# Optimization experiments

Hardware: AMD Instinct MI355X
Metric: run time of the kernel (lower is better)

Reference implementation:

```python
import jax, jax.numpy as jnp
import numpy as np

NUM_CODES = 1024
EMBED_DIM = 256
COMMITMENT_COST = 0.25


def setup_inputs() -> dict:
    key = jax.random.key(0)
    kz, kc = jax.random.split(key)
    z = jax.random.normal(kz, (131072, EMBED_DIM), dtype=jnp.float32)
    # codebook init matches nn.Embedding weight uniform_(-1/num_codes, 1/num_codes)
    codebook = jax.random.uniform(kc, (NUM_CODES, EMBED_DIM), dtype=jnp.float32,
                                  minval=-1.0 / NUM_CODES, maxval=1.0 / NUM_CODES)
    return {"z": z, "codebook": codebook}


def reference(z, codebook):
    # Squared-euclidean distances; argmin is identical to cdist (euclidean) argmin.
    z2 = jnp.sum(z * z, axis=-1, keepdims=True)            # [N, 1]
    c2 = jnp.sum(codebook * codebook, axis=-1)             # [K]
    d = z2 - 2.0 * (z @ codebook.T) + c2                   # [N, K]
    indices = jnp.argmin(d, axis=-1)                       # [N]
    zq = codebook[indices]                                 # [N, D] embedding lookup

    commitment_loss = COMMITMENT_COST * jnp.mean(
        (jax.lax.stop_gradient(zq) - z) ** 2)
    zq_st = z + jax.lax.stop_gradient(zq - z)              # straight-through
    residual = z - jax.lax.stop_gradient(zq)               # z - z_q.detach()

    counts = jnp.bincount(indices, length=NUM_CODES).astype(jnp.float32)
    avg_probs = counts / jnp.sum(counts)
    perplexity = jnp.exp(-jnp.sum(avg_probs * jnp.log(avg_probs + 1e-10)))

    return zq_st, residual, indices, commitment_loss, perplexity
```

## Files before the change

### kernel.cpp

```cpp
#include <hip/hip_runtime.h>
#include <math.h>

#define NR 131072
#define KC 1024
#define DD 256

#define ZQ_OFF  0
#define RES_OFF 33554432
#define IDX_OFF 67108864
#define LOSS_OFF 67239936
#define PERP_OFF 67239937

#define WS_CNT 0
#define WS_C2N 4096
#define WS_BSS 8192
#define WS_CBS 16384

#define MARG 5e-4f
#define CCAP 28

#define FM(x,y) __fmul_rn((x),(y))
#define FA(x,y) __fadd_rn((x),(y))

typedef __attribute__((ext_vector_type(8))) short bf16x8;
typedef __attribute__((ext_vector_type(4))) float f32x4;

static __device__ __forceinline__ unsigned short bf16h(float f) {
  unsigned int u = __float_as_uint(f);
  u += 0x7FFFu + ((u >> 16) & 1u);
  return (unsigned short)(u >> 16);
}

static __device__ __forceinline__ void glds16(const void* g, void* l) {
  __builtin_amdgcn_global_load_lds(
      (const __attribute__((address_space(1))) void*)g,
      (__attribute__((address_space(3))) void*)l, 16, 0, 0);
}

static __device__ __forceinline__ float np_sumsq128(const float* __restrict__ q) {
  float lane[16];
#pragma unroll
  for (int l = 0; l < 16; l++) {
    float s0 = FM(q[l +   0], q[l +   0]);
    float s1 = FM(q[l +  16], q[l +  16]);
    float s2 = FM(q[l +  32], q[l +  32]);
    float s3 = FM(q[l +  48], q[l +  48]);
    float s4 = FM(q[l +  64], q[l +  64]);
    float s5 = FM(q[l +  80], q[l +  80]);
    float s6 = FM(q[l +  96], q[l +  96]);
    float s7 = FM(q[l + 112], q[l + 112]);
    lane[l] = FA(FA(FA(s0, s1), FA(s2, s3)), FA(FA(s4, s5), FA(s6, s7)));
  }
#pragma unroll
  for (int h = 8; h >= 1; h >>= 1)
#pragma unroll
    for (int l = 0; l < 8; l++)
      if (l < h) lane[l] = FA(lane[l], lane[l + h]);
  return lane[0];
}

static __device__ __forceinline__ float np_sumsq256(const float* __restrict__ p) {
  return FA(np_sumsq128(p), np_sumsq128(p + 128));
}

__global__ void vqo_c2(const float* __restrict__ cb, float* __restrict__ c2n) {
  const int code = blockIdx.x * 256 + threadIdx.x;
  if (code < KC) c2n[code] = np_sumsq256(cb + (size_t)code * DD);
}

__global__ void vqo_cbsplit(const float* __restrict__ cb,
                            unsigned short* __restrict__ cbs) {
  const int g  = blockIdx.x * 256 + threadIdx.x;
  const int t  = g >> 9;
  const int gi = g & 511;
  const int kc = gi >> 6, q = (gi >> 4) & 3, c = gi & 15;
  const float* src = cb + (size_t)(t * 16 + c) * DD + kc * 32 + q * 8;
  unsigned int w[4];
#pragma unroll
  for (int p = 0; p < 4; p++)
    w[p] = (unsigned int)bf16h(src[p * 2]) |
           ((unsigned int)bf16h(src[p * 2 + 1]) << 16);
  *(uint4*)(cbs + (size_t)g * 8) = make_uint4(w[0], w[1], w[2], w[3]);
}

__global__ __launch_bounds__(256, 4) void vqo_main(
    const float* __restrict__ z, const float* __restrict__ cb,
    const unsigned short* __restrict__ cbs,
    const float* __restrict__ c2n,
    float* __restrict__ out, int* __restrict__ counts,
    double* __restrict__ bss) {
  __shared__ __align__(16) unsigned short ct[2][4096];
  __shared__ unsigned short ccode[128][CCAP];
  __shared__ float cd[128][CCAP];
  __shared__ int ccnt[128];
  __shared__ float m1row[128];
  __shared__ float z2s[128];
  __shared__ int rowidx[128];
  __shared__ double wred[4];

  const int tid = threadIdx.x, wg = blockIdx.x;
  const int wv = tid >> 6, ln = tid & 63;
  const int rl = ln & 15;
  const int qk = ln >> 4;
  const int rowg0 = wg * 128 + wv * 32 + rl;

#define STG(T, B) do {                                                        \
    _Pragma("unroll")                                                         \
    for (int u_ = 0; u_ < 2; u_++) {                                          \
      glds16(cbs + (size_t)(T) * 4096 + (size_t)((wv * 2 + u_) * 64 + ln) * 8,\
             &ct[B][(wv * 2 + u_) * 512]);                                    \
    }                                                                         \
  } while (0)

  STG(0, 0);

  bf16x8 zH0[8], zH1[8];
#pragma unroll
  for (int kc = 0; kc < 8; kc++) {
    const float4* p0 = (const float4*)(z + (size_t)rowg0 * DD + kc * 32 + qk * 8);
    const float4* p1 = (const float4*)(z + (size_t)(rowg0 + 16) * DD + kc * 32 + qk * 8);
    const float4 a0 = p0[0], b0 = p0[1];
    const float4 a1 = p1[0], b1 = p1[1];
    zH0[kc][0] = (short)bf16h(a0.x); zH0[kc][1] = (short)bf16h(a0.y);
    zH0[kc][2] = (short)bf16h(a0.z); zH0[kc][3] = (short)bf16h(a0.w);
    zH0[kc][4] = (short)bf16h(b0.x); zH0[kc][5] = (short)bf16h(b0.y);
    zH0[kc][6] = (short)bf16h(b0.z); zH0[kc][7] = (short)bf16h(b0.w);
    zH1[kc][0] = (short)bf16h(a1.x); zH1[kc][1] = (short)bf16h(a1.y);
    zH1[kc][2] = (short)bf16h(a1.z); zH1[kc][3] = (short)bf16h(a1.w);
    zH1[kc][4] = (short)bf16h(b1.x); zH1[kc][5] = (short)bf16h(b1.y);
    zH1[kc][6] = (short)bf16h(b1.z); zH1[kc][7] = (short)bf16h(b1.w);
  }

  {
    const int gg = ln >> 4, l = ln & 15;
#pragma unroll 1
    for (int g4 = 0; g4 < 8; g4++) {
      const int rlcl = wv * 32 + g4 * 4 + gg;
      const float* q = z + (size_t)(wg * 128 + rlcl) * DD;
      float blk[2];
#pragma unroll
      for (int b = 0; b < 2; b++) {
        const float* qq = q + b * 128;
        const float s0 = FM(qq[l +   0], qq[l +   0]);
        const float s1 = FM(qq[l +  16], qq[l +  16]);
        const float s2 = FM(qq[l +  32], qq[l +  32]);
        const float s3 = FM(qq[l +  48], qq[l +  48]);
        const float s4 = FM(qq[l +  64], qq[l +  64]);
        const float s5 = FM(qq[l +  80], qq[l +  80]);
        const float s6 = FM(qq[l +  96], qq[l +  96]);
        const float s7 = FM(qq[l + 112], qq[l + 112]);
        float v = FA(FA(FA(s0, s1), FA(s2, s3)), FA(FA(s4, s5), FA(s6, s7)));
#pragma unroll
        for (int h = 8; h >= 1; h >>= 1) v = FA(v, __shfl_down(v, h, 16));
        blk[b] = v;
      }
      if (l == 0) z2s[rlcl] = FA(blk[0], blk[1]);
    }
  }
  if (tid < 128) ccnt[tid] = 0;
  __syncthreads();

  const float z2v0 = z2s[wv * 32 + rl];
  const float z2v1 = z2s[wv * 32 + rl + 16];

  float m10 = INFINITY, m11 = INFINITY;
#pragma unroll 1
  for (int t = 0; t < 64; t++) {
    if (t < 63) {
      STG(t + 1, (t + 1) & 1);
      asm volatile("s_waitcnt vmcnt(2)" ::: "memory");
    } else {
      asm volatile("s_waitcnt vmcnt(0)" ::: "memory");
    }
    __builtin_amdgcn_sched_barrier(0);
    __builtin_amdgcn_s_barrier();

    const unsigned short* cbuf = ct[t & 1];
    f32x4 accA = {0.f, 0.f, 0.f, 0.f}, accB = accA;
#pragma unroll
    for (int kc = 0; kc < 8; kc++) {
      const bf16x8 aH = *(const bf16x8*)&cbuf[kc * 512 + ln * 8];
      accA = __builtin_amdgcn_mfma_f32_16x16x32_bf16(aH, zH0[kc], accA, 0, 0, 0);
      accB = __builtin_amdgcn_mfma_f32_16x16x32_bf16(aH, zH1[kc], accB, 0, 0, 0);
    }
    float dh0[4], dh1[4];
#pragma unroll
    for (int r = 0; r < 4; r++) {
      const float c2v = c2n[t * 16 + qk * 4 + r];
      dh0[r] = z2v0 - 2.f * accA[r] + c2v;
      dh1[r] = z2v1 - 2.f * accB[r] + c2v;
      m10 = fminf(m10, dh0[r]);
      m11 = fminf(m11, dh1[r]);
    }
    m10 = fminf(m10, __shfl_xor(m10, 16));
    m10 = fminf(m10, __shfl_xor(m10, 32));
    m11 = fminf(m11, __shfl_xor(m11, 16));
    m11 = fminf(m11, __shfl_xor(m11, 32));
    const int rw0 = wv * 32 + rl;
#pragma unroll
    for (int r = 0; r < 4; r++) {
      if (dh0[r] <= m10 + MARG) {
        const int s = atomicAdd(&ccnt[rw0], 1);
        if (s < CCAP) {
          ccode[rw0][s] = (unsigned short)(t * 16 + qk * 4 + r);
          cd[rw0][s] = dh0[r];
        }
      }
      if (dh1[r] <= m11 + MARG) {
        const int s = atomicAdd(&ccnt[rw0 + 16], 1);
        if (s < CCAP) {
          ccode[rw0 + 16][s] = (unsigned short)(t * 16 + qk * 4 + r);
          cd[rw0 + 16][s] = dh1[r];
        }
      }
    }
    __builtin_amdgcn_s_barrier();
  }
#undef STG

  if (qk == 0) { m1row[wv * 32 + rl] = m10; m1row[wv * 32 + rl + 16] = m11; }
  __syncthreads();

  if (tid < 128) {
    const int row = wg * 128 + tid;
    const float mf = m1row[tid] + MARG;
    const int nc = ccnt[tid];
    int best;
    if (nc > CCAP) {
      const float* zr = z + (size_t)row * DD;
      const float z2r = z2s[tid];
      float db = INFINITY; best = 0;
      for (int c = 0; c < KC; c++) {
        const float* cr = cb + (size_t)c * DD;
        float dot = 0.f;
#pragma unroll 8
        for (int k = 0; k < DD; k++) dot = __fmaf_rn(zr[k], cr[k], dot);
        const float t1 = 2.0f * dot;
        const float d = FA(FA(z2r, -t1), c2n[c]);
        if (d < db) { db = d; best = c; }
      }
    } else {
      int kept = 0, kcode = 0;
      for (int s = 0; s < nc; s++)
        if (cd[tid][s] <= mf) { kept++; kcode = ccode[tid][s]; }
      if (kept == 1) best = kcode;
      else {
        const float* zr = z + (size_t)row * DD;
        const float z2r = z2s[tid];
        float db = INFINITY; int bi = 0x7FFFFFFF;
        for (int s = 0; s < nc; s++) {
          if (cd[tid][s] > mf) continue;
          const int c = ccode[tid][s];
          const float* cr = cb + (size_t)c * DD;
          float dot = 0.f;
#pragma unroll 8
          for (int k = 0; k < DD; k++) dot = __fmaf_rn(zr[k], cr[k], dot);
          const float t1 = 2.0f * dot;
          const float d = FA(FA(z2r, -t1), c2n[c]);
          if (d < db || (d == db && c < bi)) { db = d; bi = c; }
        }
        best = bi;
      }
    }
    rowidx[tid] = best;
    atomicAdd(&counts[best], 1);
    out[IDX_OFF + row] = (float)best;
  }
  __syncthreads();

  float ss = 0.f;
#pragma unroll 1
  for (int g = 0; g < 32; g++) {
    const int rlcl = wv * 32 + g;
    const int id   = rowidx[rlcl];
    const size_t zrow = (size_t)(wg * 128 + rlcl) * DD;
    const float4 r4 = ((const float4*)(z  + zrow))[ln];
    const float4 q4 = ((const float4*)(cb + (size_t)id * DD))[ln];
    float4 stv, rsv; float dq;
    stv.x = r4.x + (q4.x - r4.x); rsv.x = r4.x - q4.x; dq = q4.x - r4.x; ss = fmaf(dq, dq, ss);
    stv.y = r4.y + (q4.y - r4.y); rsv.y = r4.y - q4.y; dq = q4.y - r4.y; ss = fmaf(dq, dq, ss);
    stv.z = r4.z + (q4.z - r4.z); rsv.z = r4.z - q4.z; dq = q4.z - r4.z; ss = fmaf(dq, dq, ss);
    stv.w = r4.w + (q4.w - r4.w); rsv.w = r4.w - q4.w; dq = q4.w - r4.w; ss = fmaf(dq, dq, ss);
    ((float4*)(out + ZQ_OFF  + zrow))[ln] = stv;
    ((float4*)(out + RES_OFF + zrow))[ln] = rsv;
  }
  double dss = (double)ss;
  for (int o = 32; o; o >>= 1) dss += __shfl_down(dss, o, 64);
  if (ln == 0) wred[wv] = dss;
  __syncthreads();
  if (tid == 0) bss[wg] = wred[0] + wred[1] + wred[2] + wred[3];
}

__global__ void vqo_final(const int* __restrict__ counts,
                          const double* __restrict__ bss,
                          float* __restrict__ out) {
  __shared__ double red[256];
  const int t = threadIdx.x;
  double s = 0.0;
  for (int i = t; i < 1024; i += 256) s += bss[i];
  red[t] = s; __syncthreads();
  for (int s2 = 128; s2 > 0; s2 >>= 1) { if (t < s2) red[t] += red[t + s2]; __syncthreads(); }
  const double ssq = red[0];
  __syncthreads();
  double h = 0.0;
  for (int c = t; c < 1024; c += 256) {
    double p = (double)counts[c] / 131072.0;
    h += p * log(p + 1e-10);
  }
  red[t] = h; __syncthreads();
  for (int s2 = 128; s2 > 0; s2 >>= 1) { if (t < s2) red[t] += red[t + s2]; __syncthreads(); }
  if (t == 0) {
    out[LOSS_OFF] = (float)(0.25 * ssq / 33554432.0);
    out[PERP_OFF] = (float)exp(-red[0]);
  }
}

extern "C" void kernel_launch(void* const* d_in, const int* in_sizes, int n_in,
                              void* d_out, int out_size, void* d_ws, size_t ws_size,
                              hipStream_t stream) {
  const float* z;
  const float* cb;
  if (in_sizes[0] == NR * DD) { z = (const float*)d_in[0]; cb = (const float*)d_in[1]; }
  else                        { cb = (const float*)d_in[0]; z = (const float*)d_in[1]; }

  float* out = (float*)d_out;
  char* ws = (char*)d_ws;
  int*            counts = (int*)(ws + WS_CNT);
  float*          c2n    = (float*)(ws + WS_C2N);
  double*         bssp   = (double*)(ws + WS_BSS);
  unsigned short* cbs    = (unsigned short*)(ws + WS_CBS);

  hipMemsetAsync(counts, 0, 4096, stream);
  vqo_c2<<<4, 256, 0, stream>>>(cb, c2n);
  vqo_cbsplit<<<128, 256, 0, stream>>>(cb, cbs);
  vqo_main<<<NR / 128, 256, 0, stream>>>(z, cb, cbs, c2n, out, counts, bssp);
  vqo_final<<<1, 256, 0, stream>>>(counts, bssp, out);
}
```

Before: 316.0 us.

## Halve rows per block to cut registers and raise occupancy

Each wave now handles 16 rows instead of 32, so each block covers 64 rows and the grid doubles to 2048 blocks. This halves the z register fragments and MFMA accumulators, and launch bounds are raised to 6 blocks per CU so more waves can hide latency. The trade-off is that every block still streams the full codebook through LDS, so codebook traffic per row doubles and each MFMA has less reuse. The candidate cap shrinks to 24 and the workspace layout moves to fit the doubled per-block partial sums.

```diff
diff --git a/kernel.cpp b/kernel.cpp
--- a/kernel.cpp
+++ b/kernel.cpp
@@ -14,10 +14,10 @@
 #define WS_CNT 0
 #define WS_C2N 4096
 #define WS_BSS 8192
-#define WS_CBS 16384
+#define WS_CBS 24576
 
 #define MARG 5e-4f
-#define CCAP 28
+#define CCAP 24
 
 #define FM(x,y) __fmul_rn((x),(y))
 #define FA(x,y) __fadd_rn((x),(y))
@@ -63,12 +63,12 @@
   return FA(np_sumsq128(p), np_sumsq128(p + 128));
 }
 
-__global__ void vqo_c2(const float* __restrict__ cb, float* __restrict__ c2n) {
+__global__ void vqp_c2(const float* __restrict__ cb, float* __restrict__ c2n) {
   const int code = blockIdx.x * 256 + threadIdx.x;
   if (code < KC) c2n[code] = np_sumsq256(cb + (size_t)code * DD);
 }
 
-__global__ void vqo_cbsplit(const float* __restrict__ cb,
+__global__ void vqp_cbsplit(const float* __restrict__ cb,
                             unsigned short* __restrict__ cbs) {
   const int g  = blockIdx.x * 256 + threadIdx.x;
   const int t  = g >> 9;
@@ -83,26 +83,27 @@
   *(uint4*)(cbs + (size_t)g * 8) = make_uint4(w[0], w[1], w[2], w[3]);
 }
 
-__global__ __launch_bounds__(256, 4) void vqo_main(
+__global__ __launch_bounds__(256, 6) void vqp_main(
     const float* __restrict__ z, const float* __restrict__ cb,
     const unsigned short* __restrict__ cbs,
     const float* __restrict__ c2n,
     float* __restrict__ out, int* __restrict__ counts,
     double* __restrict__ bss) {
   __shared__ __align__(16) unsigned short ct[2][4096];
-  __shared__ unsigned short ccode[128][CCAP];
-  __shared__ float cd[128][CCAP];
-  __shared__ int ccnt[128];
-  __shared__ float m1row[128];
-  __shared__ float z2s[128];
-  __shared__ int rowidx[128];
+  __shared__ unsigned short ccode[64][CCAP];
+  __shared__ float cd[64][CCAP];
+  __shared__ int ccnt[64];
+  __shared__ float m1row[64];
+  __shared__ float z2s[64];
+  __shared__ int rowidx[64];
   __shared__ double wred[4];
 
   const int tid = threadIdx.x, wg = blockIdx.x;
   const int wv = tid >> 6, ln = tid & 63;
   const int rl = ln & 15;
   const int qk = ln >> 4;
-  const int rowg0 = wg * 128 + wv * 32 + rl;
+  const int rw = wv * 16 + rl;
+  const int rowg = wg * 64 + rw;
 
 #define STG(T, B) do {                                                        \
     _Pragma("unroll")                                                         \
@@ -114,29 +115,23 @@
 
   STG(0, 0);
 
-  bf16x8 zH0[8], zH1[8];
+  bf16x8 zH[8];
 #pragma unroll
   for (int kc = 0; kc < 8; kc++) {
-    const float4* p0 = (const float4*)(z + (size_t)rowg0 * DD + kc * 32 + qk * 8);
-    const float4* p1 = (const float4*)(z + (size_t)(rowg0 + 16) * DD + kc * 32 + qk * 8);
+    const float4* p0 = (const float4*)(z + (size_t)rowg * DD + kc * 32 + qk * 8);
     const float4 a0 = p0[0], b0 = p0[1];
-    const float4 a1 = p1[0], b1 = p1[1];
-    zH0[kc][0] = (short)bf16h(a0.x); zH0[kc][1] = (short)bf16h(a0.y);
-    zH0[kc][2] = (short)bf16h(a0.z); zH0[kc][3] = (short)bf16h(a0.w);
-    zH0[kc][4] = (short)bf16h(b0.x); zH0[kc][5] = (short)bf16h(b0.y);
-    zH0[kc][6] = (short)bf16h(b0.z); zH0[kc][7] = (short)bf16h(b0.w);
-    zH1[kc][0] = (short)bf16h(a1.x); zH1[kc][1] = (short)bf16h(a1.y);
-    zH1[kc][2] = (short)bf16h(a1.z); zH1[kc][3] = (short)bf16h(a1.w);
-    zH1[kc][4] = (short)bf16h(b1.x); zH1[kc][5] = (short)bf16h(b1.y);
-    zH1[kc][6] = (short)bf16h(b1.z); zH1[kc][7] = (short)bf16h(b1.w);
+    zH[kc][0] = (short)bf16h(a0.x); zH[kc][1] = (short)bf16h(a0.y);
+    zH[kc][2] = (short)bf16h(a0.z); zH[kc][3] = (short)bf16h(a0.w);
+    zH[kc][4] = (short)bf16h(b0.x); zH[kc][5] = (short)bf16h(b0.y);
+    zH[kc][6] = (short)bf16h(b0.z); zH[kc][7] = (short)bf16h(b0.w);
   }
 
   {
     const int gg = ln >> 4, l = ln & 15;
 #pragma unroll 1
-    for (int g4 = 0; g4 < 8; g4++) {
-      const int rlcl = wv * 32 + g4 * 4 + gg;
-      const float* q = z + (size_t)(wg * 128 + rlcl) * DD;
+    for (int g4 = 0; g4 < 4; g4++) {
+      const int rlcl = wv * 16 + g4 * 4 + gg;
+      const float* q = z + (size_t)(wg * 64 + rlcl) * DD;
       float blk[2];
 #pragma unroll
       for (int b = 0; b < 2; b++) {
@@ -157,13 +152,12 @@
       if (l == 0) z2s[rlcl] = FA(blk[0], blk[1]);
     }
   }
-  if (tid < 128) ccnt[tid] = 0;
-  __syncthreads();
-
-  const float z2v0 = z2s[wv * 32 + rl];
-  const float z2v1 = z2s[wv * 32 + rl + 16];
-
-  float m10 = INFINITY, m11 = INFINITY;
+  if (tid < 64) ccnt[tid] = 0;
+  __syncthreads();
+
+  const float z2v = z2s[rw];
+
+  float m1 = INFINITY;
 #pragma unroll 1
   for (int t = 0; t < 64; t++) {
     if (t < 63) {
@@ -176,53 +170,40 @@
     __builtin_amdgcn_s_barrier();
 
     const unsigned short* cbuf = ct[t & 1];
-    f32x4 accA = {0.f, 0.f, 0.f, 0.f}, accB = accA;
+    f32x4 accA = {0.f, 0.f, 0.f, 0.f};
 #pragma unroll
     for (int kc = 0; kc < 8; kc++) {
       const bf16x8 aH = *(const bf16x8*)&cbuf[kc * 512 + ln * 8];
-      accA = __builtin_amdgcn_mfma_f32_16x16x32_bf16(aH, zH0[kc], accA, 0, 0, 0);
-      accB = __builtin_amdgcn_mfma_f32_16x16x32_bf16(aH, zH1[kc], accB, 0, 0, 0);
-    }
-    float dh0[4], dh1[4];
+      accA = __builtin_amdgcn_mfma_f32_16x16x32_bf16(aH, zH[kc], accA, 0, 0, 0);
+    }
+    float dh[4];
 #pragma unroll
     for (int r = 0; r < 4; r++) {
       const float c2v = c2n[t * 16 + qk * 4 + r];
-      dh0[r] = z2v0 - 2.f * accA[r] + c2v;
-      dh1[r] = z2v1 - 2.f * accB[r] + c2v;
-      m10 = fminf(m10, dh0[r]);
-      m11 = fminf(m11, dh1[r]);
-    }
-    m10 = fminf(m10, __shfl_xor(m10, 16));
-    m10 = fminf(m10, __shfl_xor(m10, 32));
-    m11 = fminf(m11, __shfl_xor(m11, 16));
-    m11 = fminf(m11, __shfl_xor(m11, 32));
-    const int rw0 = wv * 32 + rl;
+      dh[r] = z2v - 2.f * accA[r] + c2v;
+      m1 = fminf(m1, dh[r]);
+    }
+    m1 = fminf(m1, __shfl_xor(m1, 16));
+    m1 = fminf(m1, __shfl_xor(m1, 32));
 #pragma unroll
     for (int r = 0; r < 4; r++) {
-      if (dh0[r] <= m10 + MARG) {
-        const int s = atomicAdd(&ccnt[rw0], 1);
+      if (dh[r] <= m1 + MARG) {
+        const int s = atomicAdd(&ccnt[rw], 1);
         if (s < CCAP) {
-          ccode[rw0][s] = (unsigned short)(t * 16 + qk * 4 + r);
-          cd[rw0][s] = dh0[r];
+          ccode[rw][s] = (unsigned short)(t * 16 + qk * 4 + r);
+          cd[rw][s] = dh[r];
         }
       }
-      if (dh1[r] <= m11 + MARG) {
-        const int s = atomicAdd(&ccnt[rw0 + 16], 1);
-        if (s < CCAP) {
-          ccode[rw0 + 16][s] = (unsigned short)(t * 16 + qk * 4 + r);
-          cd[rw0 + 16][s] = dh1[r];
-        }
-      }
     }
     __builtin_amdgcn_s_barrier();
   }
 #undef STG
 
-  if (qk == 0) { m1row[wv * 32 + rl] = m10; m1row[wv * 32 + rl + 16] = m11; }
-  __syncthreads();
-
-  if (tid < 128) {
-    const int row = wg * 128 + tid;
+  if (qk == 0) m1row[rw] = m1;
+  __syncthreads();
+
+  if (tid < 64) {
+    const int row = wg * 64 + tid;
     const float mf = m1row[tid] + MARG;
     const int nc = ccnt[tid];
     int best;
@@ -270,10 +251,10 @@
 
   float ss = 0.f;
 #pragma unroll 1
-  for (int g = 0; g < 32; g++) {
-    const int rlcl = wv * 32 + g;
+  for (int g = 0; g < 16; g++) {
+    const int rlcl = wv * 16 + g;
     const int id   = rowidx[rlcl];
-    const size_t zrow = (size_t)(wg * 128 + rlcl) * DD;
+    const size_t zrow = (size_t)(wg * 64 + rlcl) * DD;
     const float4 r4 = ((const float4*)(z  + zrow))[ln];
     const float4 q4 = ((const float4*)(cb + (size_t)id * DD))[ln];
     float4 stv, rsv; float dq;
@@ -291,13 +272,13 @@
   if (tid == 0) bss[wg] = wred[0] + wred[1] + wred[2] + wred[3];
 }
 
-__global__ void vqo_final(const int* __restrict__ counts,
+__global__ void vqp_final(const int* __restrict__ counts,
                           const double* __restrict__ bss,
                           float* __restrict__ out) {
   __shared__ double red[256];
   const int t = threadIdx.x;
   double s = 0.0;
-  for (int i = t; i < 1024; i += 256) s += bss[i];
+  for (int i = t; i < 2048; i += 256) s += bss[i];
   red[t] = s; __syncthreads();
   for (int s2 = 128; s2 > 0; s2 >>= 1) { if (t < s2) red[t] += red[t + s2]; __syncthreads(); }
   const double ssq = red[0];
@@ -331,8 +312,8 @@
   unsigned short* cbs    = (unsigned short*)(ws + WS_CBS);
 
   hipMemsetAsync(counts, 0, 4096, stream);
-  vqo_c2<<<4, 256, 0, stream>>>(cb, c2n);
-  vqo_cbsplit<<<128, 256, 0, stream>>>(cb, cbs);
-  vqo_main<<<NR / 128, 256, 0, stream>>>(z, cb, cbs, c2n, out, counts, bssp);
-  vqo_final<<<1, 256, 0, stream>>>(counts, bssp, out);
-}
+  vqp_c2<<<4, 256, 0, stream>>>(cb, c2n);
+  vqp_cbsplit<<<128, 256, 0, stream>>>(cb, cbs);
+  vqp_main<<<NR / 64, 256, 0, stream>>>(z, cb, cbs, c2n, out, counts, bssp);
+  vqp_final<<<1, 256, 0, stream>>>(counts, bssp, out);
+}
```

After: 344.7 us. +9.1%, slower.

## Load codebook tiles directly to registers and drop LDS staging barriers

Applied to the files above, without the earlier changes.

Removes the double-buffered global_load_lds staging of the bf16 codebook tiles and the per-tile workgroup barriers. Each wave now loads its MFMA A operands straight from global (L2-resident) memory, with the loop unrolled by two so loads can overlap. The c2 norms are cached in LDS and read as a float4, and the candidate resolution is split across all four waves instead of the first 128 threads. Candidate capacity is reduced to cut LDS use. The trade-off is redundant global/L2 traffic from every wave and no explicit prefetch, and fewer candidate slots mean more rows may fall back to the full exact search.

```diff
diff --git a/kernel.cpp b/kernel.cpp
--- a/kernel.cpp
+++ b/kernel.cpp
@@ -17,7 +17,7 @@
 #define WS_CBS 16384
 
 #define MARG 5e-4f
-#define CCAP 28
+#define CCAP 24
 
 #define FM(x,y) __fmul_rn((x),(y))
 #define FA(x,y) __fadd_rn((x),(y))
@@ -29,12 +29,6 @@
   unsigned int u = __float_as_uint(f);
   u += 0x7FFFu + ((u >> 16) & 1u);
   return (unsigned short)(u >> 16);
-}
-
-static __device__ __forceinline__ void glds16(const void* g, void* l) {
-  __builtin_amdgcn_global_load_lds(
-      (const __attribute__((address_space(1))) void*)g,
-      (__attribute__((address_space(3))) void*)l, 16, 0, 0);
 }
 
 static __device__ __forceinline__ float np_sumsq128(const float* __restrict__ q) {
@@ -63,12 +57,12 @@
   return FA(np_sumsq128(p), np_sumsq128(p + 128));
 }
 
-__global__ void vqo_c2(const float* __restrict__ cb, float* __restrict__ c2n) {
+__global__ void vqq_c2(const float* __restrict__ cb, float* __restrict__ c2n) {
   const int code = blockIdx.x * 256 + threadIdx.x;
   if (code < KC) c2n[code] = np_sumsq256(cb + (size_t)code * DD);
 }
 
-__global__ void vqo_cbsplit(const float* __restrict__ cb,
+__global__ void vqq_cbsplit(const float* __restrict__ cb,
                             unsigned short* __restrict__ cbs) {
   const int g  = blockIdx.x * 256 + threadIdx.x;
   const int t  = g >> 9;
@@ -83,19 +77,19 @@
   *(uint4*)(cbs + (size_t)g * 8) = make_uint4(w[0], w[1], w[2], w[3]);
 }
 
-__global__ __launch_bounds__(256, 4) void vqo_main(
+__global__ __launch_bounds__(256, 4) void vqq_main(
     const float* __restrict__ z, const float* __restrict__ cb,
     const unsigned short* __restrict__ cbs,
     const float* __restrict__ c2n,
     float* __restrict__ out, int* __restrict__ counts,
     double* __restrict__ bss) {
-  __shared__ __align__(16) unsigned short ct[2][4096];
   __shared__ unsigned short ccode[128][CCAP];
   __shared__ float cd[128][CCAP];
   __shared__ int ccnt[128];
   __shared__ float m1row[128];
   __shared__ float z2s[128];
   __shared__ int rowidx[128];
+  __shared__ __align__(16) float c2l[1024];
   __shared__ double wred[4];
 
   const int tid = threadIdx.x, wg = blockIdx.x;
@@ -104,15 +98,7 @@
   const int qk = ln >> 4;
   const int rowg0 = wg * 128 + wv * 32 + rl;
 
-#define STG(T, B) do {                                                        \
-    _Pragma("unroll")                                                         \
-    for (int u_ = 0; u_ < 2; u_++) {                                          \
-      glds16(cbs + (size_t)(T) * 4096 + (size_t)((wv * 2 + u_) * 64 + ln) * 8,\
-             &ct[B][(wv * 2 + u_) * 512]);                                    \
-    }                                                                         \
-  } while (0)
-
-  STG(0, 0);
+  ((float4*)c2l)[tid] = ((const float4*)c2n)[tid];
 
   bf16x8 zH0[8], zH1[8];
 #pragma unroll
@@ -162,31 +148,27 @@
 
   const float z2v0 = z2s[wv * 32 + rl];
   const float z2v1 = z2s[wv * 32 + rl + 16];
+  const int rw0 = wv * 32 + rl;
 
   float m10 = INFINITY, m11 = INFINITY;
-#pragma unroll 1
+#pragma unroll 2
   for (int t = 0; t < 64; t++) {
-    if (t < 63) {
-      STG(t + 1, (t + 1) & 1);
-      asm volatile("s_waitcnt vmcnt(2)" ::: "memory");
-    } else {
-      asm volatile("s_waitcnt vmcnt(0)" ::: "memory");
-    }
-    __builtin_amdgcn_sched_barrier(0);
-    __builtin_amdgcn_s_barrier();
-
-    const unsigned short* cbuf = ct[t & 1];
+    bf16x8 aH[8];
+#pragma unroll
+    for (int kc = 0; kc < 8; kc++)
+      aH[kc] = *(const bf16x8*)(cbs + (size_t)t * 4096 + kc * 512 + ln * 8);
+
     f32x4 accA = {0.f, 0.f, 0.f, 0.f}, accB = accA;
 #pragma unroll
     for (int kc = 0; kc < 8; kc++) {
-      const bf16x8 aH = *(const bf16x8*)&cbuf[kc * 512 + ln * 8];
-      accA = __builtin_amdgcn_mfma_f32_16x16x32_bf16(aH, zH0[kc], accA, 0, 0, 0);
-      accB = __builtin_amdgcn_mfma_f32_16x16x32_bf16(aH, zH1[kc], accB, 0, 0, 0);
-    }
+      accA = __builtin_amdgcn_mfma_f32_16x16x32_bf16(aH[kc], zH0[kc], accA, 0, 0, 0);
+      accB = __builtin_amdgcn_mfma_f32_16x16x32_bf16(aH[kc], zH1[kc], accB, 0, 0, 0);
+    }
+    const float4 c2v4 = *(const float4*)&c2l[t * 16 + qk * 4];
     float dh0[4], dh1[4];
 #pragma unroll
     for (int r = 0; r < 4; r++) {
-      const float c2v = c2n[t * 16 + qk * 4 + r];
+      const float c2v = r == 0 ? c2v4.x : r == 1 ? c2v4.y : r == 2 ? c2v4.z : c2v4.w;
       dh0[r] = z2v0 - 2.f * accA[r] + c2v;
       dh1[r] = z2v1 - 2.f * accB[r] + c2v;
       m10 = fminf(m10, dh0[r]);
@@ -196,7 +178,6 @@
     m10 = fminf(m10, __shfl_xor(m10, 32));
     m11 = fminf(m11, __shfl_xor(m11, 16));
     m11 = fminf(m11, __shfl_xor(m11, 32));
-    const int rw0 = wv * 32 + rl;
 #pragma unroll
     for (int r = 0; r < 4; r++) {
       if (dh0[r] <= m10 + MARG) {
@@ -214,21 +195,20 @@
         }
       }
     }
-    __builtin_amdgcn_s_barrier();
-  }
-#undef STG
-
-  if (qk == 0) { m1row[wv * 32 + rl] = m10; m1row[wv * 32 + rl + 16] = m11; }
-  __syncthreads();
-
-  if (tid < 128) {
-    const int row = wg * 128 + tid;
-    const float mf = m1row[tid] + MARG;
-    const int nc = ccnt[tid];
+  }
+
+  if (qk == 0) { m1row[rw0] = m10; m1row[rw0 + 16] = m11; }
+  __syncthreads();
+
+  if (ln < 32) {
+    const int rwl = wv * 32 + ln;
+    const int row = wg * 128 + rwl;
+    const float mf = m1row[rwl] + MARG;
+    const int nc = ccnt[rwl];
     int best;
     if (nc > CCAP) {
       const float* zr = z + (size_t)row * DD;
-      const float z2r = z2s[tid];
+      const float z2r = z2s[rwl];
       float db = INFINITY; best = 0;
       for (int c = 0; c < KC; c++) {
         const float* cr = cb + (size_t)c * DD;
@@ -236,33 +216,33 @@
 #pragma unroll 8
         for (int k = 0; k < DD; k++) dot = __fmaf_rn(zr[k], cr[k], dot);
         const float t1 = 2.0f * dot;
-        const float d = FA(FA(z2r, -t1), c2n[c]);
+        const float d = FA(FA(z2r, -t1), c2l[c]);
         if (d < db) { db = d; best = c; }
       }
     } else {
       int kept = 0, kcode = 0;
       for (int s = 0; s < nc; s++)
-        if (cd[tid][s] <= mf) { kept++; kcode = ccode[tid][s]; }
+        if (cd[rwl][s] <= mf) { kept++; kcode = ccode[rwl][s]; }
       if (kept == 1) best = kcode;
       else {
         const float* zr = z + (size_t)row * DD;
-        const float z2r = z2s[tid];
+        const float z2r = z2s[rwl];
         float db = INFINITY; int bi = 0x7FFFFFFF;
         for (int s = 0; s < nc; s++) {
-          if (cd[tid][s] > mf) continue;
-          const int c = ccode[tid][s];
+          if (cd[rwl][s] > mf) continue;
+          const int c = ccode[rwl][s];
           const float* cr = cb + (size_t)c * DD;
           float dot = 0.f;
 #pragma unroll 8
           for (int k = 0; k < DD; k++) dot = __fmaf_rn(zr[k], cr[k], dot);
           const float t1 = 2.0f * dot;
-          const float d = FA(FA(z2r, -t1), c2n[c]);
+          const float d = FA(FA(z2r, -t1), c2l[c]);
           if (d < db || (d == db && c < bi)) { db = d; bi = c; }
         }
         best = bi;
       }
     }
-    rowidx[tid] = best;
+    rowidx[rwl] = best;
     atomicAdd(&counts[best], 1);
     out[IDX_OFF + row] = (float)best;
   }
@@ -291,7 +271,7 @@
   if (tid == 0) bss[wg] = wred[0] + wred[1] + wred[2] + wred[3];
 }
 
-__global__ void vqo_final(const int* __restrict__ counts,
+__global__ void vqq_final(const int* __restrict__ counts,
                           const double* __restrict__ bss,
                           float* __restrict__ out) {
   __shared__ double red[256];
@@ -331,8 +311,8 @@
   unsigned short* cbs    = (unsigned short*)(ws + WS_CBS);
 
   hipMemsetAsync(counts, 0, 4096, stream);
-  vqo_c2<<<4, 256, 0, stream>>>(cb, c2n);
-  vqo_cbsplit<<<128, 256, 0, stream>>>(cb, cbs);
-  vqo_main<<<NR / 128, 256, 0, stream>>>(z, cb, cbs, c2n, out, counts, bssp);
-  vqo_final<<<1, 256, 0, stream>>>(counts, bssp, out);
-}
+  vqq_c2<<<4, 256, 0, stream>>>(cb, c2n);
+  vqq_cbsplit<<<128, 256, 0, stream>>>(cb, cbs);
+  vqq_main<<<NR / 128, 256, 0, stream>>>(z, cb, cbs, c2n, out, counts, bssp);
+  vqq_final<<<1, 256, 0, stream>>>(counts, bssp, out);
+}
```

Result: no change. 320.6 us (+1.5%).
